# Kernel optimization log

Measured on AMD Instinct MI355X. Metric: run time of the kernel, lower is better.

The kernel has to match this reference:

```python
import jax, jax.numpy as jnp
import numpy as np

BETA = 0.9      # leak factor
THR = 1.0       # snntorch Leaky default threshold
ALPHA = 2.0     # snntorch ATan surrogate default alpha

@jax.custom_vjp
def spike(x):
    # Heaviside fire; surrogate gradient (ATan) on backward, as in snntorch.
    return (x > 0).astype(x.dtype)

def _spike_fwd(x):
    return spike(x), x

def _spike_bwd(x, g):
    return (g * (ALPHA / 2.0) / (1.0 + (jnp.pi / 2.0 * ALPHA * x) ** 2),)

spike.defvjp(_spike_fwd, _spike_bwd)

def setup_inputs() -> dict:
    key = jax.random.key(0)
    ks = jax.random.split(key, 7)
    B, T, I, H, O = 512, 200, 784, 128, 10
    def lin(k, fan_out, fan_in):
        bound = 1.0 / np.sqrt(fan_in)
        return jax.random.uniform(k, (fan_out, fan_in), jnp.float32, -bound, bound)
    return {
        "x": jax.random.normal(ks[0], (B, T, I), jnp.float32),
        "W1": lin(ks[1], H, I), "b1": jax.random.uniform(ks[2], (H,), jnp.float32, -1/np.sqrt(I), 1/np.sqrt(I)),
        "W2": lin(ks[3], H, H), "b2": jax.random.uniform(ks[4], (H,), jnp.float32, -1/np.sqrt(H), 1/np.sqrt(H)),
        "W3": lin(ks[5], O, H), "b3": jax.random.uniform(ks[6], (O,), jnp.float32, -1/np.sqrt(H), 1/np.sqrt(H)),
    }

def reference(x, W1, b1, W2, b2, W3, b3):
    B = x.shape[0]
    H, O = W2.shape[0], W3.shape[0]
    xt = jnp.swapaxes(x, 0, 1)  # [T, B, I] for scan over time

    def lif(cur, mem, spk_prev):
        # snntorch Leaky (reset-by-subtraction, reset computed from previous mem):
        # mem_new = beta*mem + cur - spk_prev*thr ; spk = heaviside(mem_new - thr)
        mem = BETA * mem + cur - spk_prev * THR
        return spike(mem - THR), mem

    def step(carry, inp):
        m1, s1, m2, s2, m3, s3 = carry
        s1, m1 = lif(inp @ W1.T + b1, m1, s1)
        s2, m2 = lif(s1 @ W2.T + b2, m2, s2)
        s3, m3 = lif(s2 @ W3.T + b3, m3, s3)
        return (m1, s1, m2, s2, m3, s3), s3

    z = lambda d: jnp.zeros((B, d), x.dtype)
    init = (z(H), z(H), z(H), z(H), z(O), z(O))
    _, spk_rec = jax.lax.scan(step, init, xt)
    return spk_rec  # [T, B, num_outputs], matches torch.stack(spk_rec, dim=0)
```

## Files before the change

### kernel.cpp

```cpp
#include <hip/hip_runtime.h>

namespace {
constexpr int kB = 512;
constexpr int kT = 200;
constexpr int kI = 784;
constexpr int kH = 128;
constexpr int kO = 10;
constexpr int kM = kB * kT;
constexpr float kBeta = 0.9f;
constexpr float kThr = 1.0f;
constexpr int kSplitK0 = 400;
}

template <int KSTRIDE, int SPLIT>
__global__ __launch_bounds__(128, 4) void gemm64(
    const float* __restrict__ A, const float* __restrict__ B,
    const float* __restrict__ bias, float* __restrict__ C, size_t coff) {
  constexpr int BM = 64, BK = 16;
  __shared__ float As[BK][BM + 4];
  __shared__ float Bs[BK][128 + 4];
  const int tid = threadIdx.x;
  const int tx = tid & 15;
  const int ty = tid >> 4;
  int tile, kbeg, nsteps;
  if (SPLIT) {
    tile = blockIdx.x >> 1;
    const int half = blockIdx.x & 1;
    kbeg = half ? kSplitK0 : 0;
    nsteps = half ? (KSTRIDE - kSplitK0) / BK : kSplitK0 / BK;
    if (half) C += coff;
  } else {
    tile = blockIdx.x;
    kbeg = 0;
    nsteps = KSTRIDE / BK;
  }
  const int row0 = tile * BM;

  const int ar0 = tid >> 2;
  const int ar1 = ar0 + 32;
  const int ac4 = (tid & 3) * 4;
  const int br0 = tid >> 2;
  const int bc4 = (tid & 3) * 4;

  const float* aptr0 = A + (size_t)(row0 + ar0) * KSTRIDE + kbeg + ac4;
  const float* aptr1 = A + (size_t)(row0 + ar1) * KSTRIDE + kbeg + ac4;
  const float* bptr = B + (size_t)br0 * KSTRIDE + kbeg + bc4;

  float acc[8][8];
#pragma unroll
  for (int i = 0; i < 8; ++i)
#pragma unroll
    for (int j = 0; j < 8; ++j) acc[i][j] = 0.0f;

  for (int s = 0; s < nsteps; ++s) {
    const int k0 = s * BK;
    __syncthreads();
    {
      const float4 va0 = *reinterpret_cast<const float4*>(aptr0 + k0);
      const float4 va1 = *reinterpret_cast<const float4*>(aptr1 + k0);
      As[ac4 + 0][ar0] = va0.x; As[ac4 + 1][ar0] = va0.y;
      As[ac4 + 2][ar0] = va0.z; As[ac4 + 3][ar0] = va0.w;
      As[ac4 + 0][ar1] = va1.x; As[ac4 + 1][ar1] = va1.y;
      As[ac4 + 2][ar1] = va1.z; As[ac4 + 3][ar1] = va1.w;
#pragma unroll
      for (int l = 0; l < 4; ++l) {
        const float4 vb = *reinterpret_cast<const float4*>(
            bptr + (size_t)l * 32 * KSTRIDE + k0);
        const int r = br0 + l * 32;
        Bs[bc4 + 0][r] = vb.x; Bs[bc4 + 1][r] = vb.y;
        Bs[bc4 + 2][r] = vb.z; Bs[bc4 + 3][r] = vb.w;
      }
    }
    __syncthreads();
#pragma unroll
    for (int kk = 0; kk < BK; ++kk) {
      float a[8], b[8];
      *reinterpret_cast<float4*>(&a[0]) =
          *reinterpret_cast<const float4*>(&As[kk][ty * 4]);
      *reinterpret_cast<float4*>(&a[4]) =
          *reinterpret_cast<const float4*>(&As[kk][32 + ty * 4]);
      *reinterpret_cast<float4*>(&b[0]) =
          *reinterpret_cast<const float4*>(&Bs[kk][tx * 4]);
      *reinterpret_cast<float4*>(&b[4]) =
          *reinterpret_cast<const float4*>(&Bs[kk][64 + tx * 4]);
#pragma unroll
      for (int i = 0; i < 8; ++i)
#pragma unroll
        for (int j = 0; j < 8; ++j) acc[i][j] = fmaf(a[i], b[j], acc[i][j]);
    }
  }

#pragma unroll
  for (int i = 0; i < 8; ++i) {
    const int m = (i < 4) ? (ty * 4 + i) : (32 + ty * 4 + (i - 4));
    const size_t r = (size_t)(row0 + m);
#pragma unroll
    for (int jh = 0; jh < 2; ++jh) {
      const int n = jh * 64 + tx * 4;
      float4 v;
      v.x = acc[i][jh * 4 + 0];
      v.y = acc[i][jh * 4 + 1];
      v.z = acc[i][jh * 4 + 2];
      v.w = acc[i][jh * 4 + 3];
      if (bias != nullptr) {
        v.x += bias[n + 0];
        v.y += bias[n + 1];
        v.z += bias[n + 2];
        v.w += bias[n + 3];
      }
      *reinterpret_cast<float4*>(&C[r * 128 + n]) = v;
    }
  }
}

__global__ __launch_bounds__(256) void lif_scan13(
    float* __restrict__ P0, const float* __restrict__ P1,
    const float* __restrict__ b1) {
  const int g = blockIdx.x * 256 + threadIdx.x;
  const int b = g >> 7;
  const int h = g & 127;
  const size_t base = (size_t)b * kT * 128 + h;
  const float bb = b1[h];
  float m = 0.0f, s = 0.0f;
#pragma unroll 4
  for (int t = 0; t < kT; ++t) {
    const size_t idx = base + (size_t)t * 128;
    const float cur = __fadd_rn(__fadd_rn(P0[idx], P1[idx]), bb);
    m = __fsub_rn(__fadd_rn(__fmul_rn(kBeta, m), cur), s);
    s = (m > kThr) ? 1.0f : 0.0f;
    P0[idx] = s;
  }
}

__global__ __launch_bounds__(256) void lif_scan2(float* __restrict__ buf) {
  const int g = blockIdx.x * 256 + threadIdx.x;
  const int b = g >> 7;
  const int h = g & 127;
  const size_t base = (size_t)b * kT * 128 + h;
  float m = 0.0f, s = 0.0f;
#pragma unroll 4
  for (int t = 0; t < kT; ++t) {
    const size_t idx = base + (size_t)t * 128;
    m = __fsub_rn(__fadd_rn(__fmul_rn(kBeta, m), buf[idx]), s);
    s = (m > kThr) ? 1.0f : 0.0f;
    buf[idx] = s;
  }
}

__global__ __launch_bounds__(320) void gemm3_n10(
    const float* __restrict__ A, const float* __restrict__ W3,
    const float* __restrict__ b3, float* __restrict__ C) {
  __shared__ float Ss[64][132];
  __shared__ float Ws[10][132];
  __shared__ float bs[10];
  const int tid = threadIdx.x;
  const size_t row0 = (size_t)blockIdx.x * 64;

  {
    const int r = tid >> 5;
    const int c4 = (tid & 31) * 4;
    const float4 v = *reinterpret_cast<const float4*>(&W3[r * 128 + c4]);
    Ws[r][c4 + 0] = v.x;
    Ws[r][c4 + 1] = v.y;
    Ws[r][c4 + 2] = v.z;
    Ws[r][c4 + 3] = v.w;
    if (tid < 10) bs[tid] = b3[tid];
  }
  for (int fi = tid; fi < 2048; fi += 320) {
    const int r = fi >> 5;
    const int c4 = (fi & 31) * 4;
    const float4 v =
        *reinterpret_cast<const float4*>(&A[(row0 + r) * 128 + c4]);
    Ss[r][c4 + 0] = v.x;
    Ss[r][c4 + 1] = v.y;
    Ss[r][c4 + 2] = v.z;
    Ss[r][c4 + 3] = v.w;
  }
  __syncthreads();

#pragma unroll
  for (int l = 0; l < 2; ++l) {
    const int idx = tid + l * 320;
    const int r = idx / 10;
    const int o = idx - r * 10;
    float acc = bs[o];
#pragma unroll
    for (int k = 0; k < 128; k += 4) {
      const float4 a = *reinterpret_cast<const float4*>(&Ss[r][k]);
      const float4 w = *reinterpret_cast<const float4*>(&Ws[o][k]);
      acc = fmaf(a.x, w.x, acc);
      acc = fmaf(a.y, w.y, acc);
      acc = fmaf(a.z, w.z, acc);
      acc = fmaf(a.w, w.w, acc);
    }
    C[(row0 + r) * 10 + o] = acc;
  }
}

__global__ __launch_bounds__(256) void lif_scan_out(
    const float* __restrict__ cur3, float* __restrict__ out) {
  const int g = blockIdx.x * 256 + threadIdx.x;
  if (g >= kB * kO) return;
  const int b = g / kO;
  const int o = g - b * kO;
  float m = 0.0f, s = 0.0f;
#pragma unroll 4
  for (int t = 0; t < kT; ++t) {
    const float c = cur3[((size_t)b * kT + t) * kO + o];
    m = __fsub_rn(__fadd_rn(__fmul_rn(kBeta, m), c), s);
    s = (m > kThr) ? 1.0f : 0.0f;
    out[(size_t)t * (kB * kO) + g] = s;
  }
}

extern "C" void kernel_launch(void* const* d_in, const int* in_sizes, int n_in,
                              void* d_out, int out_size, void* d_ws,
                              size_t ws_size, hipStream_t stream) {
  (void)in_sizes;
  (void)n_in;
  (void)out_size;
  (void)ws_size;
  const float* x = (const float*)d_in[0];
  const float* W1 = (const float*)d_in[1];
  const float* b1 = (const float*)d_in[2];
  const float* W2 = (const float*)d_in[3];
  const float* b2 = (const float*)d_in[4];
  const float* W3 = (const float*)d_in[5];
  const float* b3 = (const float*)d_in[6];
  float* out = (float*)d_out;

  const size_t bufElems = (size_t)kM * kH;
  float* P0 = (float*)d_ws;
  float* P1 = P0 + bufElems;

  gemm64<kI, 1><<<2 * (kM / 64), 128, 0, stream>>>(x, W1, nullptr, P0,
                                                   bufElems);
  lif_scan13<<<(kB * kH) / 256, 256, 0, stream>>>(P0, P1, b1);
  gemm64<kH, 0><<<kM / 64, 128, 0, stream>>>(P0, W2, b2, P1, 0);
  lif_scan2<<<(kB * kH) / 256, 256, 0, stream>>>(P1);
  gemm3_n10<<<kM / 64, 320, 0, stream>>>(P1, W3, b3, P0);
  lif_scan_out<<<(kB * kO + 255) / 256, 256, 0, stream>>>(P0, out);
}
```

Baseline: 403.4 us.

## Enlarge GEMM tile to 128x128 with 8x16 per-thread microtile

The FP32 SIMT GEMMs used for layers 1 and 2 now compute a 128-row block tile instead of 64, with each thread holding an 8x16 accumulator instead of 8x8. This doubles the arithmetic done per shared-memory load and halves the number of times the W tile is reloaded. The B tile in shared memory gets a skewed padding layout to avoid bank conflicts on the wider reads. In exchange, register pressure rises (occupancy hint lowered from 4 to 2), the kk loop is only partially unrolled, and the grid has half as many blocks.

```diff
diff --git a/kernel.cpp b/kernel.cpp
--- a/kernel.cpp
+++ b/kernel.cpp
@@ -13,15 +13,16 @@
 }
 
 template <int KSTRIDE, int SPLIT>
-__global__ __launch_bounds__(128, 4) void gemm64(
+__global__ __launch_bounds__(128, 2) void gemm8x16(
     const float* __restrict__ A, const float* __restrict__ B,
     const float* __restrict__ bias, float* __restrict__ C, size_t coff) {
-  constexpr int BM = 64, BK = 16;
-  __shared__ float As[BK][BM + 4];
-  __shared__ float Bs[BK][128 + 4];
+  constexpr int BM = 128, BK = 16;
+  constexpr int BROW = 160;
+  __shared__ float As[BK][132];
+  __shared__ float Bs[BK][BROW];
   const int tid = threadIdx.x;
-  const int tx = tid & 15;
-  const int ty = tid >> 4;
+  const int tn = tid & 7;
+  const int tm = tid >> 3;
   int tile, kbeg, nsteps;
   if (SPLIT) {
     tile = blockIdx.x >> 1;
@@ -36,72 +37,65 @@
   }
   const int row0 = tile * BM;
 
-  const int ar0 = tid >> 2;
-  const int ar1 = ar0 + 32;
-  const int ac4 = (tid & 3) * 4;
-  const int br0 = tid >> 2;
-  const int bc4 = (tid & 3) * 4;
-
-  const float* aptr0 = A + (size_t)(row0 + ar0) * KSTRIDE + kbeg + ac4;
-  const float* aptr1 = A + (size_t)(row0 + ar1) * KSTRIDE + kbeg + ac4;
-  const float* bptr = B + (size_t)br0 * KSTRIDE + kbeg + bc4;
-
-  float acc[8][8];
+  const int sr = tid >> 2;
+  const int sc4 = (tid & 3) * 4;
+
+  const float* aptr = A + (size_t)(row0 + sr) * KSTRIDE + kbeg + sc4;
+  const float* bptr = B + (size_t)sr * KSTRIDE + kbeg + sc4;
+
+  float acc[8][16];
 #pragma unroll
   for (int i = 0; i < 8; ++i)
 #pragma unroll
-    for (int j = 0; j < 8; ++j) acc[i][j] = 0.0f;
+    for (int j = 0; j < 16; ++j) acc[i][j] = 0.0f;
 
   for (int s = 0; s < nsteps; ++s) {
     const int k0 = s * BK;
     __syncthreads();
-    {
-      const float4 va0 = *reinterpret_cast<const float4*>(aptr0 + k0);
-      const float4 va1 = *reinterpret_cast<const float4*>(aptr1 + k0);
-      As[ac4 + 0][ar0] = va0.x; As[ac4 + 1][ar0] = va0.y;
-      As[ac4 + 2][ar0] = va0.z; As[ac4 + 3][ar0] = va0.w;
-      As[ac4 + 0][ar1] = va1.x; As[ac4 + 1][ar1] = va1.y;
-      As[ac4 + 2][ar1] = va1.z; As[ac4 + 3][ar1] = va1.w;
-#pragma unroll
-      for (int l = 0; l < 4; ++l) {
-        const float4 vb = *reinterpret_cast<const float4*>(
-            bptr + (size_t)l * 32 * KSTRIDE + k0);
-        const int r = br0 + l * 32;
-        Bs[bc4 + 0][r] = vb.x; Bs[bc4 + 1][r] = vb.y;
-        Bs[bc4 + 2][r] = vb.z; Bs[bc4 + 3][r] = vb.w;
-      }
+#pragma unroll
+    for (int l = 0; l < 4; ++l) {
+      const int r = sr + l * 32;
+      const float4 va = *reinterpret_cast<const float4*>(
+          aptr + (size_t)l * 32 * KSTRIDE + k0);
+      As[sc4 + 0][r] = va.x; As[sc4 + 1][r] = va.y;
+      As[sc4 + 2][r] = va.z; As[sc4 + 3][r] = va.w;
+      const float4 vb = *reinterpret_cast<const float4*>(
+          bptr + (size_t)l * 32 * KSTRIDE + k0);
+      const int rs = r + ((r >> 4) << 2);
+      Bs[sc4 + 0][rs] = vb.x; Bs[sc4 + 1][rs] = vb.y;
+      Bs[sc4 + 2][rs] = vb.z; Bs[sc4 + 3][rs] = vb.w;
     }
     __syncthreads();
-#pragma unroll
+#pragma unroll 4
     for (int kk = 0; kk < BK; ++kk) {
-      float a[8], b[8];
+      float a[8], b[16];
       *reinterpret_cast<float4*>(&a[0]) =
-          *reinterpret_cast<const float4*>(&As[kk][ty * 4]);
+          *reinterpret_cast<const float4*>(&As[kk][tm * 8]);
       *reinterpret_cast<float4*>(&a[4]) =
-          *reinterpret_cast<const float4*>(&As[kk][32 + ty * 4]);
-      *reinterpret_cast<float4*>(&b[0]) =
-          *reinterpret_cast<const float4*>(&Bs[kk][tx * 4]);
-      *reinterpret_cast<float4*>(&b[4]) =
-          *reinterpret_cast<const float4*>(&Bs[kk][64 + tx * 4]);
+          *reinterpret_cast<const float4*>(&As[kk][tm * 8 + 4]);
+#pragma unroll
+      for (int q = 0; q < 4; ++q)
+        *reinterpret_cast<float4*>(&b[q * 4]) =
+            *reinterpret_cast<const float4*>(&Bs[kk][tn * 20 + q * 4]);
 #pragma unroll
       for (int i = 0; i < 8; ++i)
 #pragma unroll
-        for (int j = 0; j < 8; ++j) acc[i][j] = fmaf(a[i], b[j], acc[i][j]);
+        for (int j = 0; j < 16; ++j)
+          acc[i][j] = fmaf(a[i], b[j], acc[i][j]);
     }
   }
 
 #pragma unroll
   for (int i = 0; i < 8; ++i) {
-    const int m = (i < 4) ? (ty * 4 + i) : (32 + ty * 4 + (i - 4));
-    const size_t r = (size_t)(row0 + m);
-#pragma unroll
-    for (int jh = 0; jh < 2; ++jh) {
-      const int n = jh * 64 + tx * 4;
+    const size_t r = (size_t)(row0 + tm * 8 + i);
+#pragma unroll
+    for (int q = 0; q < 4; ++q) {
+      const int n = tn * 16 + q * 4;
       float4 v;
-      v.x = acc[i][jh * 4 + 0];
-      v.y = acc[i][jh * 4 + 1];
-      v.z = acc[i][jh * 4 + 2];
-      v.w = acc[i][jh * 4 + 3];
+      v.x = acc[i][q * 4 + 0];
+      v.y = acc[i][q * 4 + 1];
+      v.z = acc[i][q * 4 + 2];
+      v.w = acc[i][q * 4 + 3];
       if (bias != nullptr) {
         v.x += bias[n + 0];
         v.y += bias[n + 1];
@@ -233,10 +227,10 @@
   float* P0 = (float*)d_ws;
   float* P1 = P0 + bufElems;
 
-  gemm64<kI, 1><<<2 * (kM / 64), 128, 0, stream>>>(x, W1, nullptr, P0,
-                                                   bufElems);
+  gemm8x16<kI, 1><<<2 * (kM / 128), 128, 0, stream>>>(x, W1, nullptr, P0,
+                                                      bufElems);
   lif_scan13<<<(kB * kH) / 256, 256, 0, stream>>>(P0, P1, b1);
-  gemm64<kH, 0><<<kM / 64, 128, 0, stream>>>(P0, W2, b2, P1, 0);
+  gemm8x16<kH, 0><<<kM / 128, 128, 0, stream>>>(P0, W2, b2, P1, 0);
   lif_scan2<<<(kB * kH) / 256, 256, 0, stream>>>(P1);
   gemm3_n10<<<kM / 64, 320, 0, stream>>>(P1, W3, b3, P0);
   lif_scan_out<<<(kB * kO + 255) / 256, 256, 0, stream>>>(P0, out);
```

Measured after the change: 498.0 us. +23.4%, slower.

## Double-buffer LDS tiles with register prefetch in the fp32 GEMM

Applied to the files above, without the earlier changes.

The tiled fp32 GEMM now keeps two LDS buffers and prefetches the next K-slice into registers while computing on the current one. This removes one barrier per K-step and hides global-load latency behind the FMA work. Launch bounds drop from 4 to 2 blocks per CU minimum, which gives the compiler more registers but may lower occupancy. LDS use per block also doubles.

```diff
diff --git a/kernel.cpp b/kernel.cpp
--- a/kernel.cpp
+++ b/kernel.cpp
@@ -12,16 +12,67 @@
 constexpr int kSplitK0 = 400;
 }
 
+__device__ __forceinline__ void gload64(float4 (&ra)[2], float4 (&rb)[4],
+                                        const float* __restrict__ aptr,
+                                        const float* __restrict__ bptr,
+                                        int KS, int k0) {
+  ra[0] = *reinterpret_cast<const float4*>(aptr + k0);
+  ra[1] = *reinterpret_cast<const float4*>(aptr + (size_t)32 * KS + k0);
+#pragma unroll
+  for (int l = 0; l < 4; ++l)
+    rb[l] = *reinterpret_cast<const float4*>(bptr + (size_t)l * 32 * KS + k0);
+}
+
+__device__ __forceinline__ void ldswrite64(float (&As)[16][68],
+                                           float (&Bs)[16][132],
+                                           const float4 (&ra)[2],
+                                           const float4 (&rb)[4], int ar0,
+                                           int ac4, int br, int bc4) {
+  As[ac4 + 0][ar0] = ra[0].x; As[ac4 + 1][ar0] = ra[0].y;
+  As[ac4 + 2][ar0] = ra[0].z; As[ac4 + 3][ar0] = ra[0].w;
+  As[ac4 + 0][ar0 + 32] = ra[1].x; As[ac4 + 1][ar0 + 32] = ra[1].y;
+  As[ac4 + 2][ar0 + 32] = ra[1].z; As[ac4 + 3][ar0 + 32] = ra[1].w;
+#pragma unroll
+  for (int l = 0; l < 4; ++l) {
+    const int r = br + l * 32;
+    Bs[bc4 + 0][r] = rb[l].x; Bs[bc4 + 1][r] = rb[l].y;
+    Bs[bc4 + 2][r] = rb[l].z; Bs[bc4 + 3][r] = rb[l].w;
+  }
+}
+
+__device__ __forceinline__ void fma64(const float (&As)[16][68],
+                                      const float (&Bs)[16][132], int ty4,
+                                      int tx4, float (&acc)[8][8]) {
+#pragma unroll
+  for (int kk = 0; kk < 16; ++kk) {
+    float a[8], b[8];
+    *reinterpret_cast<float4*>(&a[0]) =
+        *reinterpret_cast<const float4*>(&As[kk][ty4]);
+    *reinterpret_cast<float4*>(&a[4]) =
+        *reinterpret_cast<const float4*>(&As[kk][32 + ty4]);
+    *reinterpret_cast<float4*>(&b[0]) =
+        *reinterpret_cast<const float4*>(&Bs[kk][tx4]);
+    *reinterpret_cast<float4*>(&b[4]) =
+        *reinterpret_cast<const float4*>(&Bs[kk][64 + tx4]);
+#pragma unroll
+    for (int i = 0; i < 8; ++i)
+#pragma unroll
+      for (int j = 0; j < 8; ++j) acc[i][j] = fmaf(a[i], b[j], acc[i][j]);
+  }
+}
+
 template <int KSTRIDE, int SPLIT>
-__global__ __launch_bounds__(128, 4) void gemm64(
+__global__ __launch_bounds__(128, 2) void gemm64p(
     const float* __restrict__ A, const float* __restrict__ B,
     const float* __restrict__ bias, float* __restrict__ C, size_t coff) {
   constexpr int BM = 64, BK = 16;
-  __shared__ float As[BK][BM + 4];
-  __shared__ float Bs[BK][128 + 4];
+  __shared__ float As0[16][68];
+  __shared__ float Bs0[16][132];
+  __shared__ float As1[16][68];
+  __shared__ float Bs1[16][132];
   const int tid = threadIdx.x;
-  const int tx = tid & 15;
-  const int ty = tid >> 4;
+  const int tx4 = (tid & 15) * 4;
+  const int ty4 = (tid >> 4) * 4;
   int tile, kbeg, nsteps;
   if (SPLIT) {
     tile = blockIdx.x >> 1;
@@ -35,16 +86,15 @@
     nsteps = KSTRIDE / BK;
   }
   const int row0 = tile * BM;
+  const int kLast = (nsteps - 1) * BK;
 
   const int ar0 = tid >> 2;
-  const int ar1 = ar0 + 32;
   const int ac4 = (tid & 3) * 4;
-  const int br0 = tid >> 2;
+  const int br = tid >> 2;
   const int bc4 = (tid & 3) * 4;
 
-  const float* aptr0 = A + (size_t)(row0 + ar0) * KSTRIDE + kbeg + ac4;
-  const float* aptr1 = A + (size_t)(row0 + ar1) * KSTRIDE + kbeg + ac4;
-  const float* bptr = B + (size_t)br0 * KSTRIDE + kbeg + bc4;
+  const float* aptr = A + (size_t)(row0 + ar0) * KSTRIDE + kbeg + ac4;
+  const float* bptr = B + (size_t)br * KSTRIDE + kbeg + bc4;
 
   float acc[8][8];
 #pragma unroll
@@ -52,51 +102,40 @@
 #pragma unroll
     for (int j = 0; j < 8; ++j) acc[i][j] = 0.0f;
 
-  for (int s = 0; s < nsteps; ++s) {
-    const int k0 = s * BK;
+  float4 ra[2], rb[4];
+  gload64(ra, rb, aptr, bptr, KSTRIDE, 0);
+  ldswrite64(As0, Bs0, ra, rb, ar0, ac4, br, bc4);
+  gload64(ra, rb, aptr, bptr, KSTRIDE, (BK <= kLast) ? BK : kLast);
+  __syncthreads();
+
+  int s = 0;
+  while (true) {
+    fma64(As0, Bs0, ty4, tx4, acc);
+    if (s + 1 >= nsteps) break;
+    ldswrite64(As1, Bs1, ra, rb, ar0, ac4, br, bc4);
+    {
+      const int kn = ((s + 2) * BK <= kLast) ? (s + 2) * BK : kLast;
+      gload64(ra, rb, aptr, bptr, KSTRIDE, kn);
+    }
     __syncthreads();
+    fma64(As1, Bs1, ty4, tx4, acc);
+    if (s + 2 >= nsteps) break;
+    ldswrite64(As0, Bs0, ra, rb, ar0, ac4, br, bc4);
     {
-      const float4 va0 = *reinterpret_cast<const float4*>(aptr0 + k0);
-      const float4 va1 = *reinterpret_cast<const float4*>(aptr1 + k0);
-      As[ac4 + 0][ar0] = va0.x; As[ac4 + 1][ar0] = va0.y;
-      As[ac4 + 2][ar0] = va0.z; As[ac4 + 3][ar0] = va0.w;
-      As[ac4 + 0][ar1] = va1.x; As[ac4 + 1][ar1] = va1.y;
-      As[ac4 + 2][ar1] = va1.z; As[ac4 + 3][ar1] = va1.w;
-#pragma unroll
-      for (int l = 0; l < 4; ++l) {
-        const float4 vb = *reinterpret_cast<const float4*>(
-            bptr + (size_t)l * 32 * KSTRIDE + k0);
-        const int r = br0 + l * 32;
-        Bs[bc4 + 0][r] = vb.x; Bs[bc4 + 1][r] = vb.y;
-        Bs[bc4 + 2][r] = vb.z; Bs[bc4 + 3][r] = vb.w;
-      }
+      const int kn = ((s + 3) * BK <= kLast) ? (s + 3) * BK : kLast;
+      gload64(ra, rb, aptr, bptr, KSTRIDE, kn);
     }
     __syncthreads();
-#pragma unroll
-    for (int kk = 0; kk < BK; ++kk) {
-      float a[8], b[8];
-      *reinterpret_cast<float4*>(&a[0]) =
-          *reinterpret_cast<const float4*>(&As[kk][ty * 4]);
-      *reinterpret_cast<float4*>(&a[4]) =
-          *reinterpret_cast<const float4*>(&As[kk][32 + ty * 4]);
-      *reinterpret_cast<float4*>(&b[0]) =
-          *reinterpret_cast<const float4*>(&Bs[kk][tx * 4]);
-      *reinterpret_cast<float4*>(&b[4]) =
-          *reinterpret_cast<const float4*>(&Bs[kk][64 + tx * 4]);
-#pragma unroll
-      for (int i = 0; i < 8; ++i)
-#pragma unroll
-        for (int j = 0; j < 8; ++j) acc[i][j] = fmaf(a[i], b[j], acc[i][j]);
-    }
+    s += 2;
   }
 
 #pragma unroll
   for (int i = 0; i < 8; ++i) {
-    const int m = (i < 4) ? (ty * 4 + i) : (32 + ty * 4 + (i - 4));
+    const int m = (i < 4) ? (ty4 + i) : (32 + ty4 + (i - 4));
     const size_t r = (size_t)(row0 + m);
 #pragma unroll
     for (int jh = 0; jh < 2; ++jh) {
-      const int n = jh * 64 + tx * 4;
+      const int n = jh * 64 + tx4;
       float4 v;
       v.x = acc[i][jh * 4 + 0];
       v.y = acc[i][jh * 4 + 1];
@@ -233,10 +272,10 @@
   float* P0 = (float*)d_ws;
   float* P1 = P0 + bufElems;
 
-  gemm64<kI, 1><<<2 * (kM / 64), 128, 0, stream>>>(x, W1, nullptr, P0,
-                                                   bufElems);
+  gemm64p<kI, 1><<<2 * (kM / 64), 128, 0, stream>>>(x, W1, nullptr, P0,
+                                                    bufElems);
   lif_scan13<<<(kB * kH) / 256, 256, 0, stream>>>(P0, P1, b1);
-  gemm64<kH, 0><<<kM / 64, 128, 0, stream>>>(P0, W2, b2, P1, 0);
+  gemm64p<kH, 0><<<kM / 64, 128, 0, stream>>>(P0, W2, b2, P1, 0);
   lif_scan2<<<(kB * kH) / 256, 256, 0, stream>>>(P1);
   gemm3_n10<<<kM / 64, 320, 0, stream>>>(P1, W3, b3, P0);
   lif_scan_out<<<(kB * kO + 255) / 256, 256, 0, stream>>>(P0, out);
```

After: 407.8 us. About the same (+1.1%).

## Pre-transpose weights for vectorized B-tile loads and prefetch in LIF scans

Applied to the files above, without the earlier changes.

Adds a small kernel that transposes W1 and W2 into scratch space in the output buffer. The GEMMs can then load B tiles as contiguous float4 rows and store them to shared memory without scattering. The LIF scan kernels now process two neurons per thread with float2 accesses and a register prefetch pipeline four steps ahead, to hide the latency of the serial time loop. This costs two extra tiny launches and halves the thread count in the scans.

```diff
diff --git a/kernel.cpp b/kernel.cpp
--- a/kernel.cpp
+++ b/kernel.cpp
@@ -12,13 +12,24 @@
 constexpr int kSplitK0 = 400;
 }
 
+__global__ __launch_bounds__(256) void transposeW(const float* __restrict__ W,
+                                                  float* __restrict__ WT,
+                                                  int N, int K) {
+  __shared__ float t[16][17];
+  const int k0 = blockIdx.x * 16, n0 = blockIdx.y * 16;
+  const int tx = threadIdx.x & 15, ty = threadIdx.x >> 4;
+  t[ty][tx] = W[(size_t)(n0 + ty) * K + k0 + tx];
+  __syncthreads();
+  WT[(size_t)(k0 + ty) * N + n0 + tx] = t[tx][ty];
+}
+
 template <int KSTRIDE, int SPLIT>
-__global__ __launch_bounds__(128, 4) void gemm64(
-    const float* __restrict__ A, const float* __restrict__ B,
+__global__ __launch_bounds__(128, 4) void gemm64bt(
+    const float* __restrict__ A, const float* __restrict__ BT,
     const float* __restrict__ bias, float* __restrict__ C, size_t coff) {
   constexpr int BM = 64, BK = 16;
-  __shared__ float As[BK][BM + 4];
-  __shared__ float Bs[BK][128 + 4];
+  __shared__ float As[BK][68];
+  __shared__ float Bs[BK][132];
   const int tid = threadIdx.x;
   const int tx = tid & 15;
   const int ty = tid >> 4;
@@ -39,12 +50,11 @@
   const int ar0 = tid >> 2;
   const int ar1 = ar0 + 32;
   const int ac4 = (tid & 3) * 4;
-  const int br0 = tid >> 2;
-  const int bc4 = (tid & 3) * 4;
-
-  const float* aptr0 = A + (size_t)(row0 + ar0) * KSTRIDE + kbeg + ac4;
-  const float* aptr1 = A + (size_t)(row0 + ar1) * KSTRIDE + kbeg + ac4;
-  const float* bptr = B + (size_t)br0 * KSTRIDE + kbeg + bc4;
+  const int sbk = tid >> 5;
+  const int sbn4 = (tid & 31) * 4;
+
+  const float* aptr = A + (size_t)(row0 + ar0) * KSTRIDE + kbeg + ac4;
+  const float* btptr = BT + (size_t)(kbeg + sbk) * 128 + sbn4;
 
   float acc[8][8];
 #pragma unroll
@@ -56,8 +66,9 @@
     const int k0 = s * BK;
     __syncthreads();
     {
-      const float4 va0 = *reinterpret_cast<const float4*>(aptr0 + k0);
-      const float4 va1 = *reinterpret_cast<const float4*>(aptr1 + k0);
+      const float4 va0 = *reinterpret_cast<const float4*>(aptr + k0);
+      const float4 va1 = *reinterpret_cast<const float4*>(
+          aptr + (size_t)32 * KSTRIDE + k0);
       As[ac4 + 0][ar0] = va0.x; As[ac4 + 1][ar0] = va0.y;
       As[ac4 + 2][ar0] = va0.z; As[ac4 + 3][ar0] = va0.w;
       As[ac4 + 0][ar1] = va1.x; As[ac4 + 1][ar1] = va1.y;
@@ -65,10 +76,8 @@
 #pragma unroll
       for (int l = 0; l < 4; ++l) {
         const float4 vb = *reinterpret_cast<const float4*>(
-            bptr + (size_t)l * 32 * KSTRIDE + k0);
-        const int r = br0 + l * 32;
-        Bs[bc4 + 0][r] = vb.x; Bs[bc4 + 1][r] = vb.y;
-        Bs[bc4 + 2][r] = vb.z; Bs[bc4 + 3][r] = vb.w;
+            btptr + (size_t)(k0 + l * 4) * 128);
+        *reinterpret_cast<float4*>(&Bs[sbk + l * 4][sbn4]) = vb;
       }
     }
     __syncthreads();
@@ -113,38 +122,69 @@
   }
 }
 
-__global__ __launch_bounds__(256) void lif_scan13(
+#define LIF_STEP(mm, ss, curexpr)                                      \
+  {                                                                    \
+    const float cur_ = (curexpr);                                      \
+    mm = __fsub_rn(__fadd_rn(__fmul_rn(kBeta, mm), cur_), ss);         \
+    ss = (mm > kThr) ? 1.0f : 0.0f;                                    \
+  }
+
+__global__ __launch_bounds__(128) void lif_scan13(
     float* __restrict__ P0, const float* __restrict__ P1,
     const float* __restrict__ b1) {
-  const int g = blockIdx.x * 256 + threadIdx.x;
-  const int b = g >> 7;
-  const int h = g & 127;
-  const size_t base = (size_t)b * kT * 128 + h;
-  const float bb = b1[h];
-  float m = 0.0f, s = 0.0f;
-#pragma unroll 4
-  for (int t = 0; t < kT; ++t) {
-    const size_t idx = base + (size_t)t * 128;
-    const float cur = __fadd_rn(__fadd_rn(P0[idx], P1[idx]), bb);
-    m = __fsub_rn(__fadd_rn(__fmul_rn(kBeta, m), cur), s);
-    s = (m > kThr) ? 1.0f : 0.0f;
-    P0[idx] = s;
-  }
-}
-
-__global__ __launch_bounds__(256) void lif_scan2(float* __restrict__ buf) {
-  const int g = blockIdx.x * 256 + threadIdx.x;
-  const int b = g >> 7;
-  const int h = g & 127;
-  const size_t base = (size_t)b * kT * 128 + h;
-  float m = 0.0f, s = 0.0f;
-#pragma unroll 4
-  for (int t = 0; t < kT; ++t) {
-    const size_t idx = base + (size_t)t * 128;
-    m = __fsub_rn(__fadd_rn(__fmul_rn(kBeta, m), buf[idx]), s);
-    s = (m > kThr) ? 1.0f : 0.0f;
-    buf[idx] = s;
-  }
+  const int g = blockIdx.x * 128 + threadIdx.x;
+  const int b = g >> 6;
+  const int h2 = (g & 63) * 2;
+  const size_t base = (size_t)b * kT * 128 + h2;
+  const float bb0 = b1[h2], bb1 = b1[h2 + 1];
+#define LD0(t) (*reinterpret_cast<const float2*>(&P0[base + (size_t)(t)*128]))
+#define LD1(t) (*reinterpret_cast<const float2*>(&P1[base + (size_t)(t)*128]))
+  float2 cA0 = LD0(0), cA1 = LD1(0), cB0 = LD0(1), cB1 = LD1(1);
+  float2 cC0 = LD0(2), cC1 = LD1(2), cD0 = LD0(3), cD1 = LD1(3);
+  float m0 = 0.f, m1 = 0.f, s0 = 0.f, s1 = 0.f;
+  for (int t = 0; t < kT; t += 2) {
+    const int pa = (t + 4 < kT) ? t + 4 : kT - 1;
+    const int pb = (t + 5 < kT) ? t + 5 : kT - 1;
+    const float2 nA0 = LD0(pa), nA1 = LD1(pa);
+    const float2 nB0 = LD0(pb), nB1 = LD1(pb);
+    LIF_STEP(m0, s0, __fadd_rn(__fadd_rn(cA0.x, cA1.x), bb0));
+    LIF_STEP(m1, s1, __fadd_rn(__fadd_rn(cA0.y, cA1.y), bb1));
+    *reinterpret_cast<float2*>(&P0[base + (size_t)t * 128]) =
+        make_float2(s0, s1);
+    LIF_STEP(m0, s0, __fadd_rn(__fadd_rn(cB0.x, cB1.x), bb0));
+    LIF_STEP(m1, s1, __fadd_rn(__fadd_rn(cB0.y, cB1.y), bb1));
+    *reinterpret_cast<float2*>(&P0[base + (size_t)(t + 1) * 128]) =
+        make_float2(s0, s1);
+    cA0 = cC0; cA1 = cC1; cB0 = cD0; cB1 = cD1;
+    cC0 = nA0; cC1 = nA1; cD0 = nB0; cD1 = nB1;
+  }
+#undef LD0
+#undef LD1
+}
+
+__global__ __launch_bounds__(128) void lif_scan2(float* __restrict__ buf) {
+  const int g = blockIdx.x * 128 + threadIdx.x;
+  const int b = g >> 6;
+  const int h2 = (g & 63) * 2;
+  const size_t base = (size_t)b * kT * 128 + h2;
+#define LD(t) (*reinterpret_cast<const float2*>(&buf[base + (size_t)(t)*128]))
+  float2 cA = LD(0), cB = LD(1), cC = LD(2), cD = LD(3);
+  float m0 = 0.f, m1 = 0.f, s0 = 0.f, s1 = 0.f;
+  for (int t = 0; t < kT; t += 2) {
+    const int pa = (t + 4 < kT) ? t + 4 : kT - 1;
+    const int pb = (t + 5 < kT) ? t + 5 : kT - 1;
+    const float2 nA = LD(pa), nB = LD(pb);
+    LIF_STEP(m0, s0, cA.x);
+    LIF_STEP(m1, s1, cA.y);
+    *reinterpret_cast<float2*>(&buf[base + (size_t)t * 128]) =
+        make_float2(s0, s1);
+    LIF_STEP(m0, s0, cB.x);
+    LIF_STEP(m1, s1, cB.y);
+    *reinterpret_cast<float2*>(&buf[base + (size_t)(t + 1) * 128]) =
+        make_float2(s0, s1);
+    cA = cC; cB = cD; cC = nA; cD = nB;
+  }
+#undef LD
 }
 
 __global__ __launch_bounds__(320) void gemm3_n10(
@@ -233,11 +273,17 @@
   float* P0 = (float*)d_ws;
   float* P1 = P0 + bufElems;
 
-  gemm64<kI, 1><<<2 * (kM / 64), 128, 0, stream>>>(x, W1, nullptr, P0,
-                                                   bufElems);
-  lif_scan13<<<(kB * kH) / 256, 256, 0, stream>>>(P0, P1, b1);
-  gemm64<kH, 0><<<kM / 64, 128, 0, stream>>>(P0, W2, b2, P1, 0);
-  lif_scan2<<<(kB * kH) / 256, 256, 0, stream>>>(P1);
+  float* W1T = out;
+  float* W2T = W1T + (size_t)kI * kH;
+
+  transposeW<<<dim3(kI / 16, kH / 16), 256, 0, stream>>>(W1, W1T, kH, kI);
+  transposeW<<<dim3(kH / 16, kH / 16), 256, 0, stream>>>(W2, W2T, kH, kH);
+
+  gemm64bt<kI, 1><<<2 * (kM / 64), 128, 0, stream>>>(x, W1T, nullptr, P0,
+                                                     bufElems);
+  lif_scan13<<<256, 128, 0, stream>>>(P0, P1, b1);
+  gemm64bt<kH, 0><<<kM / 64, 128, 0, stream>>>(P0, W2T, b2, P1, 0);
+  lif_scan2<<<256, 128, 0, stream>>>(P1);
   gemm3_n10<<<kM / 64, 320, 0, stream>>>(P1, W3, b3, P0);
   lif_scan_out<<<(kB * kO + 255) / 256, 256, 0, stream>>>(P0, out);
 }
```

Measured after the change: 401.1 us. About the same (-0.6%).
